# Performance work log

Measured on AMD Instinct MI355X. Metric: run time of the kernel, lower is better.

Reference implementation:

```python
import jax, jax.numpy as jnp
import numpy as np

C_IN = 256
C_INTER = C_IN // 2  # max(1, C//2)
B, D, H, W = 2, 16, 64, 64


def setup_inputs() -> dict:
    key = jax.random.key(0)
    ks = jax.random.split(key, 9)
    s = 1.0 / np.sqrt(C_IN)
    si = 1.0 / np.sqrt(C_INTER)
    return {
        "x": jax.random.normal(ks[0], (B, C_IN, D, H, W), dtype=jnp.float32),
        # 1x1x1 conv weights reduce to [out, in] matrices
        "g_w": jax.random.normal(ks[1], (C_INTER, C_IN), dtype=jnp.float32) * s,
        "g_b": jax.random.normal(ks[2], (C_INTER,), dtype=jnp.float32) * s,
        "theta_w": jax.random.normal(ks[3], (C_INTER, C_IN), dtype=jnp.float32) * s,
        "theta_b": jax.random.normal(ks[4], (C_INTER,), dtype=jnp.float32) * s,
        "phi_w": jax.random.normal(ks[5], (C_INTER, C_IN), dtype=jnp.float32) * s,
        "phi_b": jax.random.normal(ks[6], (C_INTER,), dtype=jnp.float32) * s,
        # note: torch code inits W to zero; random here so gradients/outputs are non-trivial
        "W_w": jax.random.normal(ks[7], (C_IN, C_INTER), dtype=jnp.float32) * si,
        "W_b": jax.random.normal(ks[8], (C_IN,), dtype=jnp.float32) * si,
    }


def reference(x, g_w, g_b, theta_w, theta_b, phi_w, phi_b, W_w, W_b):
    b, c, d, h, w = x.shape
    n = d * h * w
    xf = x.reshape(b, c, n)  # [B, C, N]
    # 1x1x1 convs == per-position linear projections
    g = jnp.einsum('oc,bcn->bon', g_w, xf) + g_b[None, :, None]        # [B, Ci, N]
    th = jnp.einsum('oc,bcn->bon', theta_w, xf) + theta_b[None, :, None]
    ph = jnp.einsum('oc,bcn->bon', phi_w, xf) + phi_b[None, :, None]
    # f = theta^T @ phi (N x N), y = (f / N) @ g^T. Since the normalizer is a
    # constant, reassociate: kv = phi @ g^T is [Ci, Ci], avoiding the NxN matrix.
    kv = jnp.einsum('bin,bjn->bij', ph, g)                              # [B, Ci, Ci]
    y = jnp.einsum('bin,bij->bjn', th, kv) / n                          # [B, Ci, N]
    y = jnp.einsum('oc,bcn->bon', W_w, y) + W_b[None, :, None]          # [B, C, N]
    return x + y.reshape(b, c, d, h, w)
```

## Files before the change

kernel.cpp:

```cpp
#include <hip/hip_runtime.h>

#define NB 2
#define CC 256
#define CI 128
#define NN 65536
#define LDA 72
#define LDX 264

typedef __bf16 bf16x8 __attribute__((ext_vector_type(8)));
typedef float f32x4 __attribute__((ext_vector_type(4)));

__device__ __forceinline__ unsigned short f2bf(float f) {
  unsigned u = __float_as_uint(f);
  u += 0x7fffu + ((u >> 16) & 1u);
  return (unsigned short)(u >> 16);
}

__global__ __launch_bounds__(512) void nl3d_syrk2(const float* __restrict__ x,
                                                  float* __restrict__ S,
                                                  float* __restrict__ partials,
                                                  float* __restrict__ svec,
                                                  int kchunk, int use_partial) {
  __shared__ unsigned short lds[2][256 * LDA];
  const int tid = threadIdx.x;
  const int lane = tid & 63;
  const int wv = tid >> 6;
  const int wm = wv & 3, wn = wv >> 2;
  const int b = blockIdx.y;
  const int kc0 = blockIdx.x * kchunk;

  const float* xb = x + (size_t)b * CC * NN;
  f32x4 acc[4][8];
  const f32x4 zero4 = {0.f, 0.f, 0.f, 0.f};
#pragma unroll
  for (int i = 0; i < 4; ++i)
#pragma unroll
    for (int j = 0; j < 8; ++j) acc[i][j] = zero4;

  float rsum[8];
#pragma unroll
  for (int i = 0; i < 8; ++i) rsum[i] = 0.f;

  const int r0 = tid >> 4;
  const int c4 = tid & 15;
  const int m = lane & 15;
  const int kg = (lane >> 4) * 8;

  const int stages = kchunk >> 6;

  {
    float4 f[8];
#pragma unroll
    for (int i = 0; i < 8; ++i)
      f[i] = *(const float4*)(xb + (size_t)(r0 + 32 * i) * NN + kc0 + c4 * 4);
#pragma unroll
    for (int i = 0; i < 8; ++i) {
      int row = r0 + 32 * i;
      ushort4 h;
      h.x = f2bf(f[i].x); h.y = f2bf(f[i].y); h.z = f2bf(f[i].z); h.w = f2bf(f[i].w);
      *(ushort4*)&lds[0][row * LDA + c4 * 4] = h;
      rsum[i] += f[i].x + f[i].y + f[i].z + f[i].w;
    }
  }
  __syncthreads();

  int cur = 0;
  for (int s = 0; s < stages; ++s) {
    float4 g[8];
    const bool pf = (s + 1 < stages);
    if (pf) {
      const int kc = kc0 + (s + 1) * 64;
#pragma unroll
      for (int i = 0; i < 8; ++i)
        g[i] = *(const float4*)(xb + (size_t)(r0 + 32 * i) * NN + kc + c4 * 4);
    }

    const unsigned short* L = lds[cur];
#pragma unroll
    for (int kk = 0; kk < 2; ++kk) {
      bf16x8 afr[4], bfr[8];
#pragma unroll
      for (int mt = 0; mt < 4; ++mt)
        afr[mt] = *(const bf16x8*)&L[(wm * 64 + mt * 16 + m) * LDA + kk * 32 + kg];
#pragma unroll
      for (int nt = 0; nt < 8; ++nt)
        bfr[nt] = *(const bf16x8*)&L[(wn * 128 + nt * 16 + m) * LDA + kk * 32 + kg];
#pragma unroll
      for (int mt = 0; mt < 4; ++mt)
#pragma unroll
        for (int nt = 0; nt < 8; ++nt)
          acc[mt][nt] = __builtin_amdgcn_mfma_f32_16x16x32_bf16(bfr[nt], afr[mt], acc[mt][nt], 0, 0, 0);
    }

    if (pf) {
      unsigned short* Lw = (unsigned short*)lds[cur ^ 1];
#pragma unroll
      for (int i = 0; i < 8; ++i) {
        int row = r0 + 32 * i;
        ushort4 h;
        h.x = f2bf(g[i].x); h.y = f2bf(g[i].y); h.z = f2bf(g[i].z); h.w = f2bf(g[i].w);
        *(ushort4*)&Lw[row * LDA + c4 * 4] = h;
        rsum[i] += g[i].x + g[i].y + g[i].z + g[i].w;
      }
    }
    __syncthreads();
    cur ^= 1;
  }

  const int col = lane & 15;
  const int rq = (lane >> 4) * 4;
  if (use_partial) {
    float* dst = partials + ((size_t)(b * gridDim.x + blockIdx.x)) * (CC * CC);
#pragma unroll
    for (int mt = 0; mt < 4; ++mt) {
      const int gi = wm * 64 + mt * 16 + col;
#pragma unroll
      for (int nt = 0; nt < 8; ++nt) {
        const int gj = wn * 128 + nt * 16 + rq;
        float4 v;
        v.x = acc[mt][nt][0]; v.y = acc[mt][nt][1];
        v.z = acc[mt][nt][2]; v.w = acc[mt][nt][3];
        *(float4*)&dst[(size_t)gi * CC + gj] = v;
      }
    }
  } else {
    float* Sb = S + (size_t)b * CC * CC;
#pragma unroll
    for (int mt = 0; mt < 4; ++mt)
#pragma unroll
      for (int nt = 0; nt < 8; ++nt)
#pragma unroll
        for (int r = 0; r < 4; ++r) {
          int gi = wm * 64 + mt * 16 + col;
          int gj = wn * 128 + nt * 16 + rq + r;
          atomicAdd(&Sb[(size_t)gi * CC + gj], acc[mt][nt][r]);
        }
  }

  __syncthreads();
  float* ldsRS = (float*)lds[0];
  if (tid < 256) ldsRS[tid] = 0.f;
  __syncthreads();
#pragma unroll
  for (int i = 0; i < 8; ++i) atomicAdd(&ldsRS[r0 + 32 * i], rsum[i]);
  __syncthreads();
  if (tid < 256) atomicAdd(&svec[b * CC + tid], ldsRS[tid]);
}

__global__ __launch_bounds__(128) void nl3d_reduce(const float* __restrict__ partials,
                                                   float* __restrict__ S, int splits) {
  const int e = blockIdx.x * 128 + threadIdx.x;
  const int b = e >> 14;
  const int off = e & 16383;
  const float4* p = (const float4*)partials;
  float4 a0 = {0, 0, 0, 0}, a1 = {0, 0, 0, 0}, a2 = {0, 0, 0, 0}, a3 = {0, 0, 0, 0};
  const size_t base = (size_t)b * splits * 16384 + off;
  for (int s = 0; s < splits; s += 4) {
    float4 v0 = p[base + (size_t)s * 16384];
    float4 v1 = p[base + (size_t)(s + 1) * 16384];
    float4 v2 = p[base + (size_t)(s + 2) * 16384];
    float4 v3 = p[base + (size_t)(s + 3) * 16384];
    a0.x += v0.x; a0.y += v0.y; a0.z += v0.z; a0.w += v0.w;
    a1.x += v1.x; a1.y += v1.y; a1.z += v1.z; a1.w += v1.w;
    a2.x += v2.x; a2.y += v2.y; a2.z += v2.z; a2.w += v2.w;
    a3.x += v3.x; a3.y += v3.y; a3.z += v3.z; a3.w += v3.w;
  }
  float4 r;
  r.x = (a0.x + a1.x) + (a2.x + a3.x);
  r.y = (a0.y + a1.y) + (a2.y + a3.y);
  r.z = (a0.z + a1.z) + (a2.z + a3.z);
  r.w = (a0.w + a1.w) + (a2.w + a3.w);
  ((float4*)S)[e] = r;
}

__global__ __launch_bounds__(256) void nl3d_b12(const float* __restrict__ phi_w,
                                                const float* __restrict__ S,
                                                const float* __restrict__ svec,
                                                const float* __restrict__ g_w,
                                                const float* __restrict__ phi_b,
                                                const float* __restrict__ g_b,
                                                float* __restrict__ kv) {
  __shared__ float Prow[CC];
  __shared__ float svl[CC];
  const int b = blockIdx.x >> 7, i = blockIdx.x & 127;
  const int d = threadIdx.x;
  const float* Sb = S + (size_t)b * CC * CC;
  const float* ph = phi_w + i * CC;
  float a0 = 0.f, a1 = 0.f, a2 = 0.f, a3 = 0.f;
  float a4 = 0.f, a5 = 0.f, a6 = 0.f, a7 = 0.f;
  for (int c = 0; c < CC; c += 8) {
    a0 += ph[c + 0] * Sb[(c + 0) * CC + d];
    a1 += ph[c + 1] * Sb[(c + 1) * CC + d];
    a2 += ph[c + 2] * Sb[(c + 2) * CC + d];
    a3 += ph[c + 3] * Sb[(c + 3) * CC + d];
    a4 += ph[c + 4] * Sb[(c + 4) * CC + d];
    a5 += ph[c + 5] * Sb[(c + 5) * CC + d];
    a6 += ph[c + 6] * Sb[(c + 6) * CC + d];
    a7 += ph[c + 7] * Sb[(c + 7) * CC + d];
  }
  Prow[d] = ((a0 + a1) + (a2 + a3)) + ((a4 + a5) + (a6 + a7));
  svl[d] = svec[b * CC + d];
  __syncthreads();

  if (d < CI) {
    const int j = d;
    const float* gr = g_w + (size_t)j * CC;
    float p0 = 0.f, p1 = 0.f, p2 = 0.f, p3 = 0.f;
    float v0 = 0.f, v1 = 0.f, v2 = 0.f, v3 = 0.f;
    float u0 = 0.f, u1 = 0.f, u2 = 0.f, u3 = 0.f;
    for (int c = 0; c < CC; c += 4) {
      float g0 = gr[c], g1 = gr[c + 1], g2 = gr[c + 2], g3 = gr[c + 3];
      p0 += Prow[c] * g0;     p1 += Prow[c + 1] * g1;
      p2 += Prow[c + 2] * g2; p3 += Prow[c + 3] * g3;
      v0 += svl[c] * g0;      v1 += svl[c + 1] * g1;
      v2 += svl[c + 2] * g2;  v3 += svl[c + 3] * g3;
      u0 += ph[c] * svl[c];       u1 += ph[c + 1] * svl[c + 1];
      u2 += ph[c + 2] * svl[c + 2]; u3 += ph[c + 3] * svl[c + 3];
    }
    float a = (p0 + p1) + (p2 + p3);
    float v = (v0 + v1) + (v2 + v3);
    float u = (u0 + u1) + (u2 + u3);
    kv[((size_t)b * CI + i) * CI + j] =
        a + u * g_b[j] + phi_b[i] * (v + (float)NN * g_b[j]);
  }
}

__global__ void nl3d_b3(const float* __restrict__ kv, const float* __restrict__ theta_w,
                        const float* __restrict__ theta_b, float* __restrict__ T2,
                        float* __restrict__ tb2) {
  int b = blockIdx.x >> 7, j = blockIdx.x & 127, c = threadIdx.x;
  const float* kvb = kv + (size_t)b * CI * CI;
  float a0 = 0.f, a1 = 0.f, a2 = 0.f, a3 = 0.f;
  for (int i = 0; i < CI; i += 4) {
    a0 += kvb[i * CI + j] * theta_w[i * CC + c];
    a1 += kvb[(i + 1) * CI + j] * theta_w[(i + 1) * CC + c];
    a2 += kvb[(i + 2) * CI + j] * theta_w[(i + 2) * CC + c];
    a3 += kvb[(i + 3) * CI + j] * theta_w[(i + 3) * CC + c];
  }
  T2[((size_t)b * CI + j) * CC + c] = (a0 + a1) + (a2 + a3);
  if (c == 0) {
    float t = 0.f;
    for (int i = 0; i < CI; ++i) t += kvb[i * CI + j] * theta_b[i];
    tb2[b * CI + j] = t;
  }
}

__global__ void nl3d_b4(const float* __restrict__ T2, const float* __restrict__ tb2,
                        const float* __restrict__ W_w, const float* __restrict__ W_b,
                        unsigned short* __restrict__ Mbf, float* __restrict__ cvec) {
  int b = blockIdx.x >> 8, o = blockIdx.x & 255, c = threadIdx.x;
  const float inv = 1.0f / (float)NN;
  const float* Wr = W_w + o * CI;
  float a0 = 0.f, a1 = 0.f, a2 = 0.f, a3 = 0.f;
  for (int j = 0; j < CI; j += 4) {
    a0 += Wr[j] * T2[((size_t)b * CI + j) * CC + c];
    a1 += Wr[j + 1] * T2[((size_t)b * CI + j + 1) * CC + c];
    a2 += Wr[j + 2] * T2[((size_t)b * CI + j + 2) * CC + c];
    a3 += Wr[j + 3] * T2[((size_t)b * CI + j + 3) * CC + c];
  }
  Mbf[((size_t)b * CC + o) * CC + c] = f2bf(((a0 + a1) + (a2 + a3)) * inv);
  if (c == 0) {
    float t = 0.f;
    for (int j = 0; j < CI; ++j) t += Wr[j] * tb2[b * CI + j];
    cvec[b * CC + o] = t * inv + W_b[o];
  }
}

__global__ __launch_bounds__(512) void nl3d_out(const float* __restrict__ x,
                                                const unsigned short* __restrict__ Mbf,
                                                const float* __restrict__ cvec,
                                                float* __restrict__ out) {
  __shared__ unsigned short xT[64 * LDX];
  const int tid = threadIdx.x;
  const int lane = tid & 63;
  const int wv = tid >> 6;
  const int wm = wv & 3;
  const int wn = wv >> 2;
  const int b = blockIdx.y;
  const int n0 = blockIdx.x * 64;

  const float* xb = x + (size_t)b * CC * NN;
  float* ob = out + (size_t)b * CC * NN;

  {
    const int c4 = tid & 15;
    const int t4 = tid >> 4;
    float4 f0[4], f1[4];
#pragma unroll
    for (int i = 0; i < 4; ++i) {
      int p = i * 32 + t4;
      f0[i] = *(const float4*)(xb + (size_t)(2 * p) * NN + n0 + c4 * 4);
      f1[i] = *(const float4*)(xb + (size_t)(2 * p + 1) * NN + n0 + c4 * 4);
    }
#pragma unroll
    for (int i = 0; i < 4; ++i) {
      int p = i * 32 + t4;
      int ps = p ^ ((c4 & 7) << 2);
      float a0[4] = {f0[i].x, f0[i].y, f0[i].z, f0[i].w};
      float a1[4] = {f1[i].x, f1[i].y, f1[i].z, f1[i].w};
#pragma unroll
      for (int j = 0; j < 4; ++j) {
        unsigned pack = (unsigned)f2bf(a0[j]) | ((unsigned)f2bf(a1[j]) << 16);
        *(unsigned*)&xT[(c4 * 4 + j) * LDX + 2 * ps] = pack;
      }
    }
  }
  __syncthreads();

  f32x4 acc[4][2];
  const f32x4 zero4 = {0.f, 0.f, 0.f, 0.f};
#pragma unroll
  for (int i = 0; i < 4; ++i)
#pragma unroll
    for (int j = 0; j < 2; ++j) acc[i][j] = zero4;

  const int m = lane & 15;
  const int kg = (lane >> 4) * 8;
  const unsigned short* Mb = Mbf + (size_t)b * CC * CC;
#pragma unroll
  for (int kc = 0; kc < 8; ++kc) {
    bf16x8 afr[4], bfr[2];
#pragma unroll
    for (int mt = 0; mt < 4; ++mt)
      afr[mt] = *(const bf16x8*)(Mb + (size_t)(wm * 64 + mt * 16 + m) * CC + kc * 32 + kg);
#pragma unroll
    for (int nt = 0; nt < 2; ++nt) {
      int rr = wn * 32 + nt * 16 + m;
      int d0 = (kc * 16 + (kg >> 1)) ^ (((rr >> 2) & 7) << 2);
      bfr[nt] = *(const bf16x8*)&xT[rr * LDX + 2 * d0];
    }
#pragma unroll
    for (int mt = 0; mt < 4; ++mt)
#pragma unroll
      for (int nt = 0; nt < 2; ++nt)
        acc[mt][nt] = __builtin_amdgcn_mfma_f32_16x16x32_bf16(afr[mt], bfr[nt], acc[mt][nt], 0, 0, 0);
  }

  const int col = lane & 15;
  const int rquad = (lane >> 4) * 4;
#pragma unroll
  for (int mt = 0; mt < 4; ++mt)
#pragma unroll
    for (int r = 0; r < 4; ++r) {
      int o = wm * 64 + mt * 16 + rquad + r;
      float cv = cvec[b * CC + o];
      const float* xrow = xb + (size_t)o * NN + n0;
      float* orow = ob + (size_t)o * NN + n0;
#pragma unroll
      for (int nt = 0; nt < 2; ++nt) {
        int n = wn * 32 + nt * 16 + col;
        orow[n] = xrow[n] + acc[mt][nt][r] + cv;
      }
    }
}

extern "C" void kernel_launch(void* const* d_in, const int* in_sizes, int n_in,
                              void* d_out, int out_size, void* d_ws, size_t ws_size,
                              hipStream_t stream) {
  const float* x       = (const float*)d_in[0];
  const float* g_w     = (const float*)d_in[1];
  const float* g_b     = (const float*)d_in[2];
  const float* theta_w = (const float*)d_in[3];
  const float* theta_b = (const float*)d_in[4];
  const float* phi_w   = (const float*)d_in[5];
  const float* phi_b   = (const float*)d_in[6];
  const float* W_w     = (const float*)d_in[7];
  const float* W_b     = (const float*)d_in[8];
  float* out = (float*)d_out;

  char* ws = (char*)d_ws;
  float* S    = (float*)(ws);
  float* svec = (float*)(ws + 524288);
  float* kv   = (float*)(ws + 919552);
  float* T2   = (float*)(ws + 1050624);
  float* tb2  = (float*)(ws + 1312768);
  unsigned short* Mbf = (unsigned short*)(ws + 1313792);
  float* cvec = (float*)(ws + 1575936);
  float* partials = (float*)(ws + 2097152);

  int splits = 0;
  for (int c = 128; c >= 8; c >>= 1) {
    if (2097152 + (size_t)NB * c * CC * CC * 4 <= ws_size) { splits = c; break; }
  }

  if (splits > 0) {
    hipMemsetAsync(svec, 0, 2048, stream);
    nl3d_syrk2<<<dim3(splits, NB), 512, 0, stream>>>(x, S, partials, svec,
                                                     NN / splits, 1);
    nl3d_reduce<<<256, 128, 0, stream>>>(partials, S, splits);
  } else {
    hipMemsetAsync(ws, 0, 526336, stream);
    nl3d_syrk2<<<dim3(64, NB), 512, 0, stream>>>(x, S, (float*)ws, svec,
                                                 NN / 64, 0);
  }
  nl3d_b12<<<NB * CI, 256, 0, stream>>>(phi_w, S, svec, g_w, phi_b, g_b, kv);
  nl3d_b3<<<NB * CI, 256, 0, stream>>>(kv, theta_w, theta_b, T2, tb2);
  nl3d_b4<<<NB * CC, 256, 0, stream>>>(T2, tb2, W_w, W_b, Mbf, cvec);
  nl3d_out<<<dim3(NN / 64, NB), 512, 0, stream>>>(x, Mbf, cvec, out);
}
```

Baseline: 409.4 us.

## Restructure output kernel with LDS-staged coalesced epilogue and prefetched A fragments

The output GEMM kernel drops from 512 to 256 threads. Each wave now computes a 64x64 tile, and the A fragments from Mbf are prefetched one k-step ahead. The epilogue stages accumulators through LDS so that x reads and out writes become float4-coalesced rows instead of scattered scalar accesses. The partial-sum reduce kernel switches to float2 loads with 256 threads and 8-way unrolling to get more loads in flight. This adds register pressure and extra LDS barriers in the epilogue.

```diff
diff --git a/kernel.cpp b/kernel.cpp
--- a/kernel.cpp
+++ b/kernel.cpp
@@ -6,6 +6,7 @@
 #define NN 65536
 #define LDA 72
 #define LDX 264
+#define LDSW 68
 
 typedef __bf16 bf16x8 __attribute__((ext_vector_type(8)));
 typedef float f32x4 __attribute__((ext_vector_type(4)));
@@ -147,30 +148,33 @@
   if (tid < 256) atomicAdd(&svec[b * CC + tid], ldsRS[tid]);
 }
 
-__global__ __launch_bounds__(128) void nl3d_reduce(const float* __restrict__ partials,
+__global__ __launch_bounds__(256) void nl3d_reduce(const float* __restrict__ partials,
                                                    float* __restrict__ S, int splits) {
-  const int e = blockIdx.x * 128 + threadIdx.x;
-  const int b = e >> 14;
-  const int off = e & 16383;
-  const float4* p = (const float4*)partials;
-  float4 a0 = {0, 0, 0, 0}, a1 = {0, 0, 0, 0}, a2 = {0, 0, 0, 0}, a3 = {0, 0, 0, 0};
-  const size_t base = (size_t)b * splits * 16384 + off;
-  for (int s = 0; s < splits; s += 4) {
-    float4 v0 = p[base + (size_t)s * 16384];
-    float4 v1 = p[base + (size_t)(s + 1) * 16384];
-    float4 v2 = p[base + (size_t)(s + 2) * 16384];
-    float4 v3 = p[base + (size_t)(s + 3) * 16384];
-    a0.x += v0.x; a0.y += v0.y; a0.z += v0.z; a0.w += v0.w;
-    a1.x += v1.x; a1.y += v1.y; a1.z += v1.z; a1.w += v1.w;
-    a2.x += v2.x; a2.y += v2.y; a2.z += v2.z; a2.w += v2.w;
-    a3.x += v3.x; a3.y += v3.y; a3.z += v3.z; a3.w += v3.w;
-  }
-  float4 r;
-  r.x = (a0.x + a1.x) + (a2.x + a3.x);
-  r.y = (a0.y + a1.y) + (a2.y + a3.y);
-  r.z = (a0.z + a1.z) + (a2.z + a3.z);
-  r.w = (a0.w + a1.w) + (a2.w + a3.w);
-  ((float4*)S)[e] = r;
+  const int e = blockIdx.x * 256 + threadIdx.x;
+  const int b = e >> 15;
+  const int off = e & 32767;
+  const float2* p = (const float2*)partials;
+  float2 a0 = {0, 0}, a1 = {0, 0}, a2 = {0, 0}, a3 = {0, 0};
+  float2 a4 = {0, 0}, a5 = {0, 0}, a6 = {0, 0}, a7 = {0, 0};
+  const size_t base = (size_t)b * splits * 32768 + off;
+  for (int s = 0; s < splits; s += 8) {
+    float2 v0 = p[base + (size_t)(s + 0) * 32768];
+    float2 v1 = p[base + (size_t)(s + 1) * 32768];
+    float2 v2 = p[base + (size_t)(s + 2) * 32768];
+    float2 v3 = p[base + (size_t)(s + 3) * 32768];
+    float2 v4 = p[base + (size_t)(s + 4) * 32768];
+    float2 v5 = p[base + (size_t)(s + 5) * 32768];
+    float2 v6 = p[base + (size_t)(s + 6) * 32768];
+    float2 v7 = p[base + (size_t)(s + 7) * 32768];
+    a0.x += v0.x; a0.y += v0.y;  a1.x += v1.x; a1.y += v1.y;
+    a2.x += v2.x; a2.y += v2.y;  a3.x += v3.x; a3.y += v3.y;
+    a4.x += v4.x; a4.y += v4.y;  a5.x += v5.x; a5.y += v5.y;
+    a6.x += v6.x; a6.y += v6.y;  a7.x += v7.x; a7.y += v7.y;
+  }
+  float2 r;
+  r.x = ((a0.x + a1.x) + (a2.x + a3.x)) + ((a4.x + a5.x) + (a6.x + a7.x));
+  r.y = ((a0.y + a1.y) + (a2.y + a3.y)) + ((a4.y + a5.y) + (a6.y + a7.y));
+  ((float2*)S)[e] = r;
 }
 
 __global__ __launch_bounds__(256) void nl3d_b12(const float* __restrict__ phi_w,
@@ -266,16 +270,15 @@
   }
 }
 
-__global__ __launch_bounds__(512) void nl3d_out(const float* __restrict__ x,
+__global__ __launch_bounds__(256) void nl3d_out(const float* __restrict__ x,
                                                 const unsigned short* __restrict__ Mbf,
                                                 const float* __restrict__ cvec,
                                                 float* __restrict__ out) {
-  __shared__ unsigned short xT[64 * LDX];
+  __shared__ __align__(16) char smem[128 * LDSW * 4];
+  unsigned short* xT = (unsigned short*)smem;
   const int tid = threadIdx.x;
   const int lane = tid & 63;
   const int wv = tid >> 6;
-  const int wm = wv & 3;
-  const int wn = wv >> 2;
   const int b = blockIdx.y;
   const int n0 = blockIdx.x * 64;
 
@@ -285,16 +288,16 @@
   {
     const int c4 = tid & 15;
     const int t4 = tid >> 4;
-    float4 f0[4], f1[4];
-#pragma unroll
-    for (int i = 0; i < 4; ++i) {
-      int p = i * 32 + t4;
+    float4 f0[8], f1[8];
+#pragma unroll
+    for (int i = 0; i < 8; ++i) {
+      int p = i * 16 + t4;
       f0[i] = *(const float4*)(xb + (size_t)(2 * p) * NN + n0 + c4 * 4);
       f1[i] = *(const float4*)(xb + (size_t)(2 * p + 1) * NN + n0 + c4 * 4);
     }
 #pragma unroll
-    for (int i = 0; i < 4; ++i) {
-      int p = i * 32 + t4;
+    for (int i = 0; i < 8; ++i) {
+      int p = i * 16 + t4;
       int ps = p ^ ((c4 & 7) << 2);
       float a0[4] = {f0[i].x, f0[i].y, f0[i].z, f0[i].w};
       float a1[4] = {f1[i].x, f1[i].y, f1[i].z, f1[i].w};
@@ -307,51 +310,79 @@
   }
   __syncthreads();
 
-  f32x4 acc[4][2];
+  f32x4 acc[4][4];
   const f32x4 zero4 = {0.f, 0.f, 0.f, 0.f};
 #pragma unroll
   for (int i = 0; i < 4; ++i)
 #pragma unroll
-    for (int j = 0; j < 2; ++j) acc[i][j] = zero4;
+    for (int j = 0; j < 4; ++j) acc[i][j] = zero4;
 
   const int m = lane & 15;
   const int kg = (lane >> 4) * 8;
   const unsigned short* Mb = Mbf + (size_t)b * CC * CC;
+
+  bf16x8 afr[4];
+#pragma unroll
+  for (int mt = 0; mt < 4; ++mt)
+    afr[mt] = *(const bf16x8*)(Mb + (size_t)(wv * 64 + mt * 16 + m) * CC + kg);
 #pragma unroll
   for (int kc = 0; kc < 8; ++kc) {
-    bf16x8 afr[4], bfr[2];
-#pragma unroll
-    for (int mt = 0; mt < 4; ++mt)
-      afr[mt] = *(const bf16x8*)(Mb + (size_t)(wm * 64 + mt * 16 + m) * CC + kc * 32 + kg);
-#pragma unroll
-    for (int nt = 0; nt < 2; ++nt) {
-      int rr = wn * 32 + nt * 16 + m;
+    bf16x8 curf[4];
+#pragma unroll
+    for (int mt = 0; mt < 4; ++mt) curf[mt] = afr[mt];
+    if (kc < 7) {
+#pragma unroll
+      for (int mt = 0; mt < 4; ++mt)
+        afr[mt] = *(const bf16x8*)(Mb + (size_t)(wv * 64 + mt * 16 + m) * CC + (kc + 1) * 32 + kg);
+    }
+    bf16x8 bfr[4];
+#pragma unroll
+    for (int nt = 0; nt < 4; ++nt) {
+      int rr = nt * 16 + m;
       int d0 = (kc * 16 + (kg >> 1)) ^ (((rr >> 2) & 7) << 2);
       bfr[nt] = *(const bf16x8*)&xT[rr * LDX + 2 * d0];
     }
 #pragma unroll
     for (int mt = 0; mt < 4; ++mt)
 #pragma unroll
-      for (int nt = 0; nt < 2; ++nt)
-        acc[mt][nt] = __builtin_amdgcn_mfma_f32_16x16x32_bf16(afr[mt], bfr[nt], acc[mt][nt], 0, 0, 0);
-  }
-
-  const int col = lane & 15;
-  const int rquad = (lane >> 4) * 4;
-#pragma unroll
-  for (int mt = 0; mt < 4; ++mt)
-#pragma unroll
-    for (int r = 0; r < 4; ++r) {
-      int o = wm * 64 + mt * 16 + rquad + r;
-      float cv = cvec[b * CC + o];
-      const float* xrow = xb + (size_t)o * NN + n0;
-      float* orow = ob + (size_t)o * NN + n0;
-#pragma unroll
-      for (int nt = 0; nt < 2; ++nt) {
-        int n = wn * 32 + nt * 16 + col;
-        orow[n] = xrow[n] + acc[mt][nt][r] + cv;
-      }
-    }
+      for (int nt = 0; nt < 4; ++nt)
+        acc[mt][nt] = __builtin_amdgcn_mfma_f32_16x16x32_bf16(curf[mt], bfr[nt], acc[mt][nt], 0, 0, 0);
+  }
+
+  float* eb = (float*)smem;
+  const int colo = lane & 15;
+  const int rq4 = (lane >> 4) * 4;
+  const int frow = lane >> 4;
+  const int fcol = (lane & 15) * 4;
+#pragma unroll
+  for (int h = 0; h < 2; ++h) {
+    __syncthreads();
+#pragma unroll
+    for (int mi = 0; mi < 2; ++mi) {
+      const int mt = 2 * h + mi;
+      const int lrb = wv * 32 + mi * 16 + rq4;
+#pragma unroll
+      for (int nt = 0; nt < 4; ++nt)
+#pragma unroll
+        for (int r = 0; r < 4; ++r)
+          eb[(lrb + r) * LDSW + nt * 16 + colo] = acc[mt][nt][r];
+    }
+    __syncthreads();
+#pragma unroll
+    for (int it = 0; it < 8; ++it) {
+      const int lr = wv * 32 + it * 4 + frow;
+      const int o  = wv * 64 + h * 32 + it * 4 + frow;
+      float4 v = *(float4*)&eb[lr * LDSW + fcol];
+      const float cv = cvec[b * CC + o];
+      float4 xv = *(const float4*)(xb + (size_t)o * NN + n0 + fcol);
+      float4 rr;
+      rr.x = xv.x + v.x + cv;
+      rr.y = xv.y + v.y + cv;
+      rr.z = xv.z + v.z + cv;
+      rr.w = xv.w + v.w + cv;
+      *(float4*)(ob + (size_t)o * NN + n0 + fcol) = rr;
+    }
+  }
 }
 
 extern "C" void kernel_launch(void* const* d_in, const int* in_sizes, int n_in,
@@ -387,7 +418,7 @@
     hipMemsetAsync(svec, 0, 2048, stream);
     nl3d_syrk2<<<dim3(splits, NB), 512, 0, stream>>>(x, S, partials, svec,
                                                      NN / splits, 1);
-    nl3d_reduce<<<256, 128, 0, stream>>>(partials, S, splits);
+    nl3d_reduce<<<256, 256, 0, stream>>>(partials, S, splits);
   } else {
     hipMemsetAsync(ws, 0, 526336, stream);
     nl3d_syrk2<<<dim3(64, NB), 512, 0, stream>>>(x, S, (float*)ws, svec,
@@ -396,5 +427,5 @@
   nl3d_b12<<<NB * CI, 256, 0, stream>>>(phi_w, S, svec, g_w, phi_b, g_b, kv);
   nl3d_b3<<<NB * CI, 256, 0, stream>>>(kv, theta_w, theta_b, T2, tb2);
   nl3d_b4<<<NB * CC, 256, 0, stream>>>(T2, tb2, W_w, W_b, Mbf, cvec);
-  nl3d_out<<<dim3(NN / 64, NB), 512, 0, stream>>>(x, Mbf, cvec, out);
-}
+  nl3d_out<<<dim3(NN / 64, NB), 256, 0, stream>>>(x, Mbf, cvec, out);
+}
```

Result: faster. 381.3 us (-6.9%).
